# Performance work log

Measured on AMD Instinct MI355X. Metric: run time of the kernel, lower is better.

Reference implementation:

```python
import jax, jax.numpy as jnp
import numpy as np

N = 2_000_000   # n_nodes
D = 8           # manifold_dim
C = 1.0         # hyperbolic curvature

# ---- Poincare ball ops (curvature C), vectorized over leading node axis ----
def _hyp_proj(x, eps=1e-5):
    norm = jnp.linalg.norm(x, axis=-1, keepdims=True)
    max_norm = (1.0 - eps) / jnp.sqrt(C)
    return jnp.where(norm > max_norm, x / norm * max_norm, x)

def _mobius_add(x, y):
    xy = jnp.sum(x * y, axis=-1, keepdims=True)
    nx = jnp.sum(x ** 2, axis=-1, keepdims=True)
    ny = jnp.sum(y ** 2, axis=-1, keepdims=True)
    num = (1.0 + 2.0 * C * xy + C * ny) * x + (1.0 - C * nx) * y
    den = 1.0 + 2.0 * C * xy + C ** 2 * nx * ny
    return num / (den + 1e-10)

def _hyp_exp(x, v):
    nv = jnp.maximum(jnp.linalg.norm(v, axis=-1, keepdims=True), 1e-10)
    sc = jnp.sqrt(C)
    nx = jnp.linalg.norm(x, axis=-1, keepdims=True)
    lam = 2.0 / (1.0 - C * nx ** 2)
    coef = jnp.tanh(sc * lam * nv / 2) / (sc * nv)
    return _hyp_proj(_mobius_add(x, coef * v))

def _hyp_log(x, y):
    sub = _mobius_add(-x, y)
    ns = jnp.maximum(jnp.linalg.norm(sub, axis=-1, keepdims=True), 1e-10)
    sc = jnp.sqrt(C)
    nx = jnp.linalg.norm(x, axis=-1, keepdims=True)
    lam = 2.0 / (1.0 - C * nx ** 2)
    coef = jnp.arctanh(sc * ns) / (sc * ns * lam / 2)
    return coef * sub

# ---- sphere ops ----
def _sph_proj(x):
    return x / (jnp.linalg.norm(x, axis=-1, keepdims=True) + 1e-10)

def _sph_log(x, y):
    xy = jnp.clip(jnp.sum(x * y, axis=-1, keepdims=True), -1.0 + 1e-6, 1.0 - 1e-6)
    coef = jnp.arccos(xy) / jnp.sqrt(1.0 - xy ** 2 + 1e-10)
    return coef * (y - xy * x)

def _sph_exp(x, v):
    nv = jnp.maximum(jnp.linalg.norm(v, axis=-1, keepdims=True), 1e-10)
    return _sph_proj(jnp.cos(nv) * x + jnp.sin(nv) * v / nv)


def setup_inputs() -> dict:
    key = jax.random.key(0)
    ks = jax.random.split(key, 9)
    f32 = jnp.float32
    return {
        'features': jax.random.normal(ks[0], (N, 8), dtype=f32),
        # flax Dense default init ~ lecun_normal: std = 1/sqrt(fan_in)
        'W_hyp': jax.random.normal(ks[1], (2, D), dtype=f32) / np.sqrt(2.0),
        'b_hyp': jnp.zeros((D,), dtype=f32),
        'W_spd': jax.random.normal(ks[2], (3, 3), dtype=f32) / np.sqrt(3.0),
        'b_spd': jnp.zeros((3,), dtype=f32),
        'W_sph': jax.random.normal(ks[3], (2, D), dtype=f32) / np.sqrt(2.0),
        'b_sph': jnp.zeros((D,), dtype=f32),
        'W_int': jax.random.normal(ks[4], (4 + D + 3 + D, 32), dtype=f32) / np.sqrt(4.0 + D + 3 + D),
        'b_int': jnp.zeros((32,), dtype=f32),
    }


def reference(features, W_hyp, b_hyp, W_spd, b_spd, W_sph, b_sph, W_int, b_int):
    euclid = features[:, :4]            # [N,4]
    mf = features[:, 4:]                # [N,4] manifold features

    # --- hyperbolic branch: exp-map of MLP output at the origin ---
    hyp_tan = mf[:, 0:2] @ W_hyp + b_hyp            # [N,D]
    hyp_pt = _hyp_exp(jnp.zeros_like(hyp_tan), hyp_tan)

    # --- SPD branch: matrices are diag(exp(Dense(feat)) + 0.1) ---
    spd_diag = jnp.exp(mf[:, 0:3] @ W_spd + b_spd) + 0.1   # [N,3]

    # --- sphere branch ---
    sph_pt = _sph_proj(mf[:, 2:4] @ W_sph + b_sph)          # [N,D]

    # --- geodesic refinement: hyperbolic ---
    hc = _hyp_proj(jnp.mean(hyp_pt, axis=0, keepdims=True))
    hyp_ref = _hyp_exp(hyp_pt, 0.1 * _hyp_log(hyp_pt, hc))

    # --- geodesic refinement: SPD ---
    # matrices and centroid are diagonal, so (1-a)*M + a*centroid is diagonal;
    # eigh + clamp + reconstruct of a diagonal SPD matrix == diag(max(d, 1e-6))
    geo_mean = jnp.exp(jnp.mean(jnp.log(spd_diag + 1e-8), axis=0))   # [3]
    spd_ref_diag = jnp.maximum(0.9 * spd_diag + 0.1 * geo_mean, 1e-6)  # [N,3]
    spd_ref = jnp.eye(3, dtype=spd_ref_diag.dtype) * spd_ref_diag[:, None, :]  # [N,3,3]

    # --- geodesic refinement: sphere ---
    sc = _sph_proj(jnp.mean(sph_pt, axis=0, keepdims=True))
    sph_ref = _sph_exp(sph_pt, 0.1 * _sph_log(sph_pt, sc))

    # --- pullbacks to tangent space + integration ---
    hyp_pull = _hyp_log(jnp.zeros_like(hyp_ref), hyp_ref)
    spd_pull = jnp.log(spd_ref_diag + 1e-8)
    combined = jnp.concatenate([euclid, hyp_pull, spd_pull, sph_ref], axis=-1)  # [N,23]
    integrated = jax.nn.relu(combined @ W_int + b_int)    # [N,32]
    return (integrated, hyp_ref, spd_ref, sph_ref, combined)
```

## Files before the change

### kernel.cpp

```cpp
#include <hip/hip_runtime.h>
#include <math.h>

#define NB1 1024
#define BS  256

typedef float f4v __attribute__((ext_vector_type(4)));

__device__ __forceinline__ void nts4(float4* p, float4 v) {
    __builtin_nontemporal_store(*(const f4v*)&v, (f4v*)p);
}
__device__ __forceinline__ void nts1(float* p, float v) {
    __builtin_nontemporal_store(v, p);
}

__device__ __forceinline__ void compute_base(
    const float4 mf,
    const float* __restrict__ Wh, const float* __restrict__ bh,
    const float* __restrict__ Ws, const float* __restrict__ bs,
    const float* __restrict__ Wp, const float* __restrict__ bp,
    float* hp, float* sd, float* sp)
{
    float ht[8];
    float nv2 = 0.f;
#pragma unroll
    for (int j = 0; j < 8; ++j) {
        float t = mf.x * Wh[j] + mf.y * Wh[8 + j] + bh[j];
        ht[j] = t; nv2 += t * t;
    }
    float nv = fmaxf(sqrtf(nv2), 1e-10f);
    float coef = tanhf(nv) / nv;
    float pn2 = 0.f;
#pragma unroll
    for (int j = 0; j < 8; ++j) {
        float p = coef * ht[j];
        hp[j] = p; pn2 += p * p;
    }
    float pn = sqrtf(pn2);
    if (pn > 0.99999f) {
        float s = 0.99999f / pn;
#pragma unroll
        for (int j = 0; j < 8; ++j) hp[j] *= s;
    }
#pragma unroll
    for (int k = 0; k < 3; ++k) {
        float t = mf.x * Ws[k] + mf.y * Ws[3 + k] + mf.z * Ws[6 + k] + bs[k];
        sd[k] = expf(t) + 0.1f;
    }
    float sl[8]; float sn2 = 0.f;
#pragma unroll
    for (int j = 0; j < 8; ++j) {
        float t = mf.z * Wp[j] + mf.w * Wp[8 + j] + bp[j];
        sl[j] = t; sn2 += t * t;
    }
    float isn = 1.0f / (sqrtf(sn2) + 1e-10f);
#pragma unroll
    for (int j = 0; j < 8; ++j) sp[j] = sl[j] * isn;
}

__global__ __launch_bounds__(BS) void reduce_kernel(
    const float* __restrict__ feat, int n,
    const float* __restrict__ Wh, const float* __restrict__ bh,
    const float* __restrict__ Ws, const float* __restrict__ bs,
    const float* __restrict__ Wp, const float* __restrict__ bp,
    float* __restrict__ partials)
{
    float acc[19];
#pragma unroll
    for (int i = 0; i < 19; ++i) acc[i] = 0.f;
    int stride = gridDim.x * blockDim.x;
    for (int row = blockIdx.x * blockDim.x + threadIdx.x; row < n; row += stride) {
        float4 mf = *(const float4*)(feat + (size_t)row * 8 + 4);
        float hp[8], sd[3], sp[8];
        compute_base(mf, Wh, bh, Ws, bs, Wp, bp, hp, sd, sp);
#pragma unroll
        for (int j = 0; j < 8; ++j) acc[j] += hp[j];
#pragma unroll
        for (int k = 0; k < 3; ++k) acc[8 + k] += logf(sd[k] + 1e-8f);
#pragma unroll
        for (int j = 0; j < 8; ++j) acc[11 + j] += sp[j];
    }
#pragma unroll
    for (int i = 0; i < 19; ++i) {
#pragma unroll
        for (int off = 32; off >= 1; off >>= 1)
            acc[i] += __shfl_down(acc[i], off, 64);
    }
    __shared__ float red[4][19];
    int lane = threadIdx.x & 63, wid = threadIdx.x >> 6;
    if (lane == 0) {
#pragma unroll
        for (int i = 0; i < 19; ++i) red[wid][i] = acc[i];
    }
    __syncthreads();
    if (threadIdx.x < 19) {
        float s = red[0][threadIdx.x] + red[1][threadIdx.x] +
                  red[2][threadIdx.x] + red[3][threadIdx.x];
        partials[(size_t)blockIdx.x * 19 + threadIdx.x] = s;
    }
}

__global__ void finalize_kernel(const float* __restrict__ partials,
                                float* __restrict__ cons, int n)
{
    __shared__ double ms[19];
    int tid = threadIdx.x;
    int k = tid >> 3, w = tid & 7;
    if (k < 19) {
        double s = 0.0;
        for (int b = w; b < NB1; b += 8) s += (double)partials[(size_t)b * 19 + k];
#pragma unroll
        for (int off = 4; off >= 1; off >>= 1) s += __shfl_down(s, off, 8);
        if (w == 0) ms[k] = s / (double)n;
    }
    __syncthreads();
    if (tid == 0) {
        double hn2 = 0.0;
        for (int j = 0; j < 8; ++j) hn2 += ms[j] * ms[j];
        double hn = sqrt(hn2);
        double sch = (hn > 0.99999) ? (0.99999 / hn) : 1.0;
        for (int j = 0; j < 8; ++j) cons[j] = (float)(ms[j] * sch);
        for (int kk = 0; kk < 3; ++kk) cons[8 + kk] = (float)exp(ms[8 + kk]);
        double sn2 = 0.0;
        for (int j = 0; j < 8; ++j) sn2 += ms[11 + j] * ms[11 + j];
        double sn = sqrt(sn2) + 1e-10;
        for (int j = 0; j < 8; ++j) cons[11 + j] = (float)(ms[11 + j] / sn);
    }
}

__global__ __launch_bounds__(BS) void main_kernel(
    const float* __restrict__ feat, int n,
    const float* __restrict__ Wh, const float* __restrict__ bh,
    const float* __restrict__ Ws, const float* __restrict__ bs,
    const float* __restrict__ Wp, const float* __restrict__ bp,
    const float* __restrict__ cons,
    const float* __restrict__ Wi, const float* __restrict__ bi,
    float* __restrict__ out)
{
    __shared__ float4 sbuf4[8 * 257];
    __shared__ float  swi[736];
    __shared__ float  sbi[32];
    float* sf = (float*)sbuf4;

    const int tid = threadIdx.x;
    const int blockStart = blockIdx.x * BS;
    const int row = blockStart + tid;
    const bool valid = row < n;
    const int vr = min(BS, n - blockStart);

    for (int i = tid; i < 184; i += BS)
        ((float4*)swi)[i] = ((const float4*)Wi)[i];
    if (tid < 8) ((float4*)sbi)[tid] = ((const float4*)bi)[tid];

    float* out_int = out;
    float* out_hyp = out + (size_t)n * 32;
    float* out_spd = out + (size_t)n * 40;
    float* out_sph = out + (size_t)n * 49;
    float* out_cmb = out + (size_t)n * 57;

    float comb[23], hr[8], srd[3], sr[8];

    if (valid) {
        size_t r = (size_t)row;
        float4 eu = *(const float4*)(feat + r * 8);
        float4 mf = *(const float4*)(feat + r * 8 + 4);

        float p[8], sd[3], sp[8];
        compute_base(mf, Wh, bh, Ws, bs, Wp, bp, p, sd, sp);

        float hc[8];
#pragma unroll
        for (int j = 0; j < 8; ++j) hc[j] = cons[j];
        float nx2 = 0.f;
#pragma unroll
        for (int j = 0; j < 8; ++j) nx2 += p[j] * p[j];
        float xy = 0.f, ny2 = 0.f;
#pragma unroll
        for (int j = 0; j < 8; ++j) { xy -= p[j] * hc[j]; ny2 += hc[j] * hc[j]; }
        float a1 = 1.f + 2.f * xy + ny2;
        float b1 = 1.f - nx2;
        float id1 = 1.f / (1.f + 2.f * xy + nx2 * ny2 + 1e-10f);
        float sub[8]; float ns2 = 0.f;
#pragma unroll
        for (int j = 0; j < 8; ++j) {
            float s = (a1 * (-p[j]) + b1 * hc[j]) * id1;
            sub[j] = s; ns2 += s * s;
        }
        float ns  = fmaxf(sqrtf(ns2), 1e-10f);
        float lam = 2.f / (1.f - nx2);
        float vcoef = 0.1f * atanhf(ns) / (ns * lam * 0.5f);
        float v[8]; float nv2 = 0.f;
#pragma unroll
        for (int j = 0; j < 8; ++j) { float t = vcoef * sub[j]; v[j] = t; nv2 += t * t; }
        float nvv = fmaxf(sqrtf(nv2), 1e-10f);
        float ecoef = tanhf(lam * nvv * 0.5f) / nvv;
        float y[8]; float xy2 = 0.f, nyy2 = 0.f;
#pragma unroll
        for (int j = 0; j < 8; ++j) { float t = ecoef * v[j]; y[j] = t; xy2 += p[j] * t; nyy2 += t * t; }
        float a2 = 1.f + 2.f * xy2 + nyy2;
        float b2 = 1.f - nx2;
        float id2 = 1.f / (1.f + 2.f * xy2 + nx2 * nyy2 + 1e-10f);
        float hn2 = 0.f;
#pragma unroll
        for (int j = 0; j < 8; ++j) { float t = (a2 * p[j] + b2 * y[j]) * id2; hr[j] = t; hn2 += t * t; }
        float hn = sqrtf(hn2);
        if (hn > 0.99999f) {
            float s = 0.99999f / hn;
#pragma unroll
            for (int j = 0; j < 8; ++j) hr[j] *= s;
        }
        float nsb2 = 0.f;
#pragma unroll
        for (int j = 0; j < 8; ++j) nsb2 += hr[j] * hr[j];
        float nsb = fmaxf(sqrtf(nsb2), 1e-10f);
        float pcoef = atanhf(nsb) / nsb;

        float scv[8], geo3[3];
#pragma unroll
        for (int j = 0; j < 8; ++j) scv[j] = cons[11 + j];
#pragma unroll
        for (int k = 0; k < 3; ++k) geo3[k] = cons[8 + k];
        float sxy = 0.f;
#pragma unroll
        for (int j = 0; j < 8; ++j) sxy += sp[j] * scv[j];
        sxy = fminf(fmaxf(sxy, -1.f + 1e-6f), 1.f - 1e-6f);
        float svcoef = 0.1f * acosf(sxy) / sqrtf(1.f - sxy * sxy + 1e-10f);
        float sv[8]; float snv2 = 0.f;
#pragma unroll
        for (int j = 0; j < 8; ++j) { float t = svcoef * (scv[j] - sxy * sp[j]); sv[j] = t; snv2 += t * t; }
        float snv = fmaxf(sqrtf(snv2), 1e-10f);
        float cn  = cosf(snv);
        float sn_ = sinf(snv) / snv;
        float st[8]; float stn2 = 0.f;
#pragma unroll
        for (int j = 0; j < 8; ++j) { float t = cn * sp[j] + sn_ * sv[j]; st[j] = t; stn2 += t * t; }
        float istn = 1.f / (sqrtf(stn2) + 1e-10f);
#pragma unroll
        for (int j = 0; j < 8; ++j) sr[j] = st[j] * istn;

#pragma unroll
        for (int k = 0; k < 3; ++k)
            srd[k] = fmaxf(0.9f * sd[k] + 0.1f * geo3[k], 1e-6f);

        comb[0] = eu.x; comb[1] = eu.y; comb[2] = eu.z; comb[3] = eu.w;
#pragma unroll
        for (int j = 0; j < 8; ++j) comb[4 + j] = pcoef * hr[j];
#pragma unroll
        for (int k = 0; k < 3; ++k) comb[12 + k] = logf(srd[k] + 1e-8f);
#pragma unroll
        for (int j = 0; j < 8; ++j) comb[15 + j] = sr[j];
    }

    __syncthreads();

    if (valid) {
#pragma unroll
        for (int c4 = 0; c4 < 8; ++c4) {
            float a_[4];
#pragma unroll
            for (int jj = 0; jj < 4; ++jj) {
                int j = c4 * 4 + jj;
                float acc = sbi[j];
#pragma unroll
                for (int k2 = 0; k2 < 23; ++k2) acc += comb[k2] * swi[k2 * 32 + j];
                a_[jj] = fmaxf(acc, 0.f);
            }
            sbuf4[c4 * 257 + tid] = make_float4(a_[0], a_[1], a_[2], a_[3]);
        }
    }
    __syncthreads();
    {
        float4* dst4 = (float4*)(out_int + (size_t)blockStart * 32);
        const int E4 = vr * 8;
        for (int i4 = tid; i4 < E4; i4 += BS)
            nts4(dst4 + i4, sbuf4[(i4 & 7) * 257 + (i4 >> 3)]);
    }
    __syncthreads();

    if (valid) {
        float* lrow = sf + tid * 23;
#pragma unroll
        for (int k = 0; k < 23; ++k) lrow[k] = comb[k];
    }
    __syncthreads();
    {
        float* dst = out_cmb + (size_t)blockStart * 23;
        const int E = vr * 23;
        const int E4 = E >> 2;
        float4* dst4 = (float4*)dst;
        for (int i4 = tid; i4 < E4; i4 += BS)
            nts4(dst4 + i4, ((const float4*)sf)[i4]);
        for (int i = (E4 << 2) + tid; i < E; i += BS)
            nts1(dst + i, sf[i]);
    }
    __syncthreads();

    if (valid) {
        float* ls = sf + tid * 9;
        ls[0] = srd[0]; ls[1] = 0.f;    ls[2] = 0.f;
        ls[3] = 0.f;    ls[4] = srd[1]; ls[5] = 0.f;
        ls[6] = 0.f;    ls[7] = 0.f;    ls[8] = srd[2];
        sbuf4[576 + 0 * 257 + tid]  = make_float4(hr[0], hr[1], hr[2], hr[3]);
        sbuf4[576 + 1 * 257 + tid]  = make_float4(hr[4], hr[5], hr[6], hr[7]);
        sbuf4[1090 + 0 * 257 + tid] = make_float4(sr[0], sr[1], sr[2], sr[3]);
        sbuf4[1090 + 1 * 257 + tid] = make_float4(sr[4], sr[5], sr[6], sr[7]);
    }
    __syncthreads();
    {
        float* d1 = out_spd + (size_t)blockStart * 9;
        const int E = vr * 9;
        const int E4 = E >> 2;
        float4* d14 = (float4*)d1;
        for (int i4 = tid; i4 < E4; i4 += BS)
            nts4(d14 + i4, ((const float4*)sf)[i4]);
        for (int i = (E4 << 2) + tid; i < E; i += BS)
            nts1(d1 + i, sf[i]);

        float4* d24 = (float4*)(out_hyp + (size_t)blockStart * 8);
        const int H4 = vr * 2;
        for (int i4 = tid; i4 < H4; i4 += BS)
            nts4(d24 + i4, sbuf4[576 + (i4 & 1) * 257 + (i4 >> 1)]);

        float4* d34 = (float4*)(out_sph + (size_t)blockStart * 8);
        for (int i4 = tid; i4 < H4; i4 += BS)
            nts4(d34 + i4, sbuf4[1090 + (i4 & 1) * 257 + (i4 >> 1)]);
    }
}

extern "C" void kernel_launch(void* const* d_in, const int* in_sizes, int n_in,
                              void* d_out, int out_size, void* d_ws, size_t ws_size,
                              hipStream_t stream) {
    const float* feat = (const float*)d_in[0];
    const float* Wh = (const float*)d_in[1];
    const float* bh = (const float*)d_in[2];
    const float* Ws = (const float*)d_in[3];
    const float* bs = (const float*)d_in[4];
    const float* Wp = (const float*)d_in[5];
    const float* bp = (const float*)d_in[6];
    const float* Wi = (const float*)d_in[7];
    const float* bi = (const float*)d_in[8];
    int n = in_sizes[0] / 8;

    float* partials = (float*)d_ws;
    float* cons = partials + NB1 * 19;
    float* out = (float*)d_out;

    reduce_kernel<<<NB1, BS, 0, stream>>>(feat, n, Wh, bh, Ws, bs, Wp, bp, partials);
    finalize_kernel<<<1, 256, 0, stream>>>(partials, cons, n);
    main_kernel<<<(n + BS - 1) / BS, BS, 0, stream>>>(feat, n, Wh, bh, Ws, bs, Wp, bp,
                                                      cons, Wi, bi, out);
}
```

Baseline: 712.5 us.

## Split main kernel into geometry and integration kernels, use fast intrinsics

The fused main kernel is split into a geometry kernel, which writes the combined features with cached stores, and a separate integration kernel. The integration kernel reads those features back, applies the 23x32 linear layer plus ReLU, and writes the output in two half-block passes through shared memory. The aim is lower register and LDS pressure per kernel, so occupancy rises. tanh, atanh, exp, log, sin and cos are also replaced by fast intrinsics, which costs some accuracy and adds an extra global round trip of the combined tensor.

```diff
diff --git a/kernel.cpp b/kernel.cpp
--- a/kernel.cpp
+++ b/kernel.cpp
@@ -11,6 +11,14 @@
 }
 __device__ __forceinline__ void nts1(float* p, float v) {
     __builtin_nontemporal_store(v, p);
+}
+
+__device__ __forceinline__ float fast_tanh_pos(float x) {
+    float e = __expf(-2.f * x);
+    return (1.f - e) / (1.f + e);
+}
+__device__ __forceinline__ float fast_atanh01(float x) {
+    return 0.5f * __logf((1.f + x) / (1.f - x));
 }
 
 __device__ __forceinline__ void compute_base(
@@ -28,7 +36,7 @@
         ht[j] = t; nv2 += t * t;
     }
     float nv = fmaxf(sqrtf(nv2), 1e-10f);
-    float coef = tanhf(nv) / nv;
+    float coef = fast_tanh_pos(nv) / nv;
     float pn2 = 0.f;
 #pragma unroll
     for (int j = 0; j < 8; ++j) {
@@ -44,7 +52,7 @@
 #pragma unroll
     for (int k = 0; k < 3; ++k) {
         float t = mf.x * Ws[k] + mf.y * Ws[3 + k] + mf.z * Ws[6 + k] + bs[k];
-        sd[k] = expf(t) + 0.1f;
+        sd[k] = __expf(t) + 0.1f;
     }
     float sl[8]; float sn2 = 0.f;
 #pragma unroll
@@ -75,7 +83,7 @@
 #pragma unroll
         for (int j = 0; j < 8; ++j) acc[j] += hp[j];
 #pragma unroll
-        for (int k = 0; k < 3; ++k) acc[8 + k] += logf(sd[k] + 1e-8f);
+        for (int k = 0; k < 3; ++k) acc[8 + k] += __logf(sd[k] + 1e-8f);
 #pragma unroll
         for (int j = 0; j < 8; ++j) acc[11 + j] += sp[j];
     }
@@ -127,18 +135,15 @@
     }
 }
 
-__global__ __launch_bounds__(BS) void main_kernel(
+__global__ __launch_bounds__(BS) void geom_kernel(
     const float* __restrict__ feat, int n,
     const float* __restrict__ Wh, const float* __restrict__ bh,
     const float* __restrict__ Ws, const float* __restrict__ bs,
     const float* __restrict__ Wp, const float* __restrict__ bp,
     const float* __restrict__ cons,
-    const float* __restrict__ Wi, const float* __restrict__ bi,
     float* __restrict__ out)
 {
-    __shared__ float4 sbuf4[8 * 257];
-    __shared__ float  swi[736];
-    __shared__ float  sbi[32];
+    __shared__ float4 sbuf4[1604];
     float* sf = (float*)sbuf4;
 
     const int tid = threadIdx.x;
@@ -147,11 +152,6 @@
     const bool valid = row < n;
     const int vr = min(BS, n - blockStart);
 
-    for (int i = tid; i < 184; i += BS)
-        ((float4*)swi)[i] = ((const float4*)Wi)[i];
-    if (tid < 8) ((float4*)sbi)[tid] = ((const float4*)bi)[tid];
-
-    float* out_int = out;
     float* out_hyp = out + (size_t)n * 32;
     float* out_spd = out + (size_t)n * 40;
     float* out_sph = out + (size_t)n * 49;
@@ -187,12 +187,12 @@
         }
         float ns  = fmaxf(sqrtf(ns2), 1e-10f);
         float lam = 2.f / (1.f - nx2);
-        float vcoef = 0.1f * atanhf(ns) / (ns * lam * 0.5f);
+        float vcoef = 0.1f * fast_atanh01(ns) / (ns * lam * 0.5f);
         float v[8]; float nv2 = 0.f;
 #pragma unroll
         for (int j = 0; j < 8; ++j) { float t = vcoef * sub[j]; v[j] = t; nv2 += t * t; }
         float nvv = fmaxf(sqrtf(nv2), 1e-10f);
-        float ecoef = tanhf(lam * nvv * 0.5f) / nvv;
+        float ecoef = fast_tanh_pos(lam * nvv * 0.5f) / nvv;
         float y[8]; float xy2 = 0.f, nyy2 = 0.f;
 #pragma unroll
         for (int j = 0; j < 8; ++j) { float t = ecoef * v[j]; y[j] = t; xy2 += p[j] * t; nyy2 += t * t; }
@@ -212,7 +212,7 @@
 #pragma unroll
         for (int j = 0; j < 8; ++j) nsb2 += hr[j] * hr[j];
         float nsb = fmaxf(sqrtf(nsb2), 1e-10f);
-        float pcoef = atanhf(nsb) / nsb;
+        float pcoef = fast_atanh01(nsb) / nsb;
 
         float scv[8], geo3[3];
 #pragma unroll
@@ -228,8 +228,8 @@
 #pragma unroll
         for (int j = 0; j < 8; ++j) { float t = svcoef * (scv[j] - sxy * sp[j]); sv[j] = t; snv2 += t * t; }
         float snv = fmaxf(sqrtf(snv2), 1e-10f);
-        float cn  = cosf(snv);
-        float sn_ = sinf(snv) / snv;
+        float cn  = __cosf(snv);
+        float sn_ = __sinf(snv) / snv;
         float st[8]; float stn2 = 0.f;
 #pragma unroll
         for (int j = 0; j < 8; ++j) { float t = cn * sp[j] + sn_ * sv[j]; st[j] = t; stn2 += t * t; }
@@ -245,36 +245,10 @@
 #pragma unroll
         for (int j = 0; j < 8; ++j) comb[4 + j] = pcoef * hr[j];
 #pragma unroll
-        for (int k = 0; k < 3; ++k) comb[12 + k] = logf(srd[k] + 1e-8f);
+        for (int k = 0; k < 3; ++k) comb[12 + k] = __logf(srd[k] + 1e-8f);
 #pragma unroll
         for (int j = 0; j < 8; ++j) comb[15 + j] = sr[j];
     }
-
-    __syncthreads();
-
-    if (valid) {
-#pragma unroll
-        for (int c4 = 0; c4 < 8; ++c4) {
-            float a_[4];
-#pragma unroll
-            for (int jj = 0; jj < 4; ++jj) {
-                int j = c4 * 4 + jj;
-                float acc = sbi[j];
-#pragma unroll
-                for (int k2 = 0; k2 < 23; ++k2) acc += comb[k2] * swi[k2 * 32 + j];
-                a_[jj] = fmaxf(acc, 0.f);
-            }
-            sbuf4[c4 * 257 + tid] = make_float4(a_[0], a_[1], a_[2], a_[3]);
-        }
-    }
-    __syncthreads();
-    {
-        float4* dst4 = (float4*)(out_int + (size_t)blockStart * 32);
-        const int E4 = vr * 8;
-        for (int i4 = tid; i4 < E4; i4 += BS)
-            nts4(dst4 + i4, sbuf4[(i4 & 7) * 257 + (i4 >> 3)]);
-    }
-    __syncthreads();
 
     if (valid) {
         float* lrow = sf + tid * 23;
@@ -288,9 +262,9 @@
         const int E4 = E >> 2;
         float4* dst4 = (float4*)dst;
         for (int i4 = tid; i4 < E4; i4 += BS)
-            nts4(dst4 + i4, ((const float4*)sf)[i4]);
+            dst4[i4] = ((const float4*)sf)[i4];
         for (int i = (E4 << 2) + tid; i < E; i += BS)
-            nts1(dst + i, sf[i]);
+            dst[i] = sf[i];
     }
     __syncthreads();
 
@@ -323,6 +297,71 @@
         float4* d34 = (float4*)(out_sph + (size_t)blockStart * 8);
         for (int i4 = tid; i4 < H4; i4 += BS)
             nts4(d34 + i4, sbuf4[1090 + (i4 & 1) * 257 + (i4 >> 1)]);
+    }
+}
+
+__global__ __launch_bounds__(BS) void int_kernel(
+    int n,
+    const float* __restrict__ Wi, const float* __restrict__ bi,
+    float* __restrict__ out)
+{
+    __shared__ float4 b4[1472];
+    float* bf = (float*)b4;
+
+    const int tid = threadIdx.x;
+    const int blockStart = blockIdx.x * BS;
+    const int row = blockStart + tid;
+    const bool valid = row < n;
+    const int vr = min(BS, n - blockStart);
+
+    float* out_int = out;
+    const float* out_cmb = out + (size_t)n * 57;
+
+    {
+        const float* src = out_cmb + (size_t)blockStart * 23;
+        const int E = vr * 23;
+        const int E4 = E >> 2;
+        const float4* src4 = (const float4*)src;
+        for (int i4 = tid; i4 < E4; i4 += BS) b4[i4] = src4[i4];
+        for (int i = (E4 << 2) + tid; i < E; i += BS) bf[i] = src[i];
+    }
+    __syncthreads();
+
+    float o[32];
+    if (valid) {
+        float c[23];
+#pragma unroll
+        for (int k = 0; k < 23; ++k) c[k] = bf[tid * 23 + k];
+#pragma unroll
+        for (int j = 0; j < 32; ++j) o[j] = bi[j];
+#pragma unroll
+        for (int k = 0; k < 23; ++k) {
+            float ck = c[k];
+#pragma unroll
+            for (int j = 0; j < 32; ++j)
+                o[j] += ck * Wi[k * 32 + j];
+        }
+#pragma unroll
+        for (int j = 0; j < 32; ++j) o[j] = fmaxf(o[j], 0.f);
+    }
+
+#pragma unroll
+    for (int h = 0; h < 2; ++h) {
+        __syncthreads();
+        if (valid && (tid >> 7) == h) {
+            int t = tid & 127;
+#pragma unroll
+            for (int c4 = 0; c4 < 8; ++c4)
+                b4[c4 * 129 + t] = make_float4(o[c4 * 4], o[c4 * 4 + 1],
+                                               o[c4 * 4 + 2], o[c4 * 4 + 3]);
+        }
+        __syncthreads();
+        int rows = vr - h * 128;
+        rows = rows < 0 ? 0 : (rows > 128 ? 128 : rows);
+        float4* dst4 = (float4*)(out_int + (size_t)(blockStart + h * 128) * 32);
+        const int E4 = rows * 8;
+        for (int i4 = tid; i4 < E4; i4 += BS)
+            nts4(dst4 + i4, b4[(i4 & 7) * 129 + (i4 >> 3)]);
     }
 }
 
@@ -344,8 +383,9 @@
     float* cons = partials + NB1 * 19;
     float* out = (float*)d_out;
 
+    int nb = (n + BS - 1) / BS;
     reduce_kernel<<<NB1, BS, 0, stream>>>(feat, n, Wh, bh, Ws, bs, Wp, bp, partials);
     finalize_kernel<<<1, 256, 0, stream>>>(partials, cons, n);
-    main_kernel<<<(n + BS - 1) / BS, BS, 0, stream>>>(feat, n, Wh, bh, Ws, bs, Wp, bp,
-                                                      cons, Wi, bi, out);
-}
+    geom_kernel<<<nb, BS, 0, stream>>>(feat, n, Wh, bh, Ws, bs, Wp, bp, cons, out);
+    int_kernel<<<nb, BS, 0, stream>>>(n, Wi, bi, out);
+}
```

New measurement: 750.4 us. +5.3%, slower.
